# Optimization experiments

Measured on AMD Instinct MI355X. Metric: run time of the kernel, lower is better.

Reference implementation:

```python
import jax, jax.numpy as jnp
import numpy as np

L, B, N, D, H, DH, MLP = 4, 4, 2048, 512, 8, 64, 2048
EPS = 1e-5


def layer_norm(x, w, b):
    mu = jnp.mean(x, axis=-1, keepdims=True)
    var = jnp.mean(jnp.square(x - mu), axis=-1, keepdims=True)
    return (x - mu) * jax.lax.rsqrt(var + EPS) * w + b


def setup_inputs() -> dict:
    key = jax.random.key(0)
    ks = jax.random.split(key, 8)
    x = jax.random.normal(ks[0], (B, N, D), dtype=jnp.float32)
    # mask == 1.0 means blocked: triu(ones) - eye -> strict upper triangle
    mask = jnp.triu(jnp.ones((N, N), dtype=jnp.float32)) - jnp.eye(N, dtype=jnp.float32)
    s = 0.02
    return {
        "x": x,
        "mask": mask,
        "ln1_w": jnp.ones((L, D), jnp.float32),
        "ln1_b": jnp.zeros((L, D), jnp.float32),
        "w_qkv": jax.random.normal(ks[1], (L, D, 3 * H * DH), jnp.float32) * s,
        "w_out": jax.random.normal(ks[2], (L, H * DH, D), jnp.float32) * s,
        "b_out": jnp.zeros((L, D), jnp.float32),
        "ln2_w": jnp.ones((L, D), jnp.float32),
        "ln2_b": jnp.zeros((L, D), jnp.float32),
        "w1": jax.random.normal(ks[3], (L, D, MLP), jnp.float32) * s,
        "b1": jnp.zeros((L, MLP), jnp.float32),
        "w2": jax.random.normal(ks[4], (L, MLP, D), jnp.float32) * s,
        "b2": jnp.zeros((L, D), jnp.float32),
    }


def reference(x, mask, ln1_w, ln1_b, w_qkv, w_out, b_out, ln2_w, ln2_b, w1, b1, w2, b2):
    scale = DH ** (-0.5)
    blocked = (mask == 1.0)  # [N, N]
    for l in range(L):
        # --- masked self-attention (pre-norm) ---
        h = layer_norm(x, ln1_w[l], ln1_b[l])
        qkv = h @ w_qkv[l]                               # [B, N, 3*H*DH]
        q, k, v = jnp.split(qkv, 3, axis=-1)
        q = q.reshape(B, N, H, DH).transpose(0, 2, 1, 3)  # bhnd
        k = k.reshape(B, N, H, DH).transpose(0, 2, 1, 3)
        v = v.reshape(B, N, H, DH).transpose(0, 2, 1, 3)
        scores = jnp.einsum('bhnd,bhmd->bhnm', q, k) * scale
        scores = jnp.where(blocked, -jnp.inf, scores)
        att = jax.nn.softmax(scores, axis=-1)
        o = jnp.einsum('bhnm,bhmd->bhnd', att, v)
        o = o.transpose(0, 2, 1, 3).reshape(B, N, H * DH)
        x = x + (o @ w_out[l] + b_out[l])
        # --- GELU MLP (pre-norm) ---
        h2 = layer_norm(x, ln2_w[l], ln2_b[l])
        ff = jax.nn.gelu(h2 @ w1[l] + b1[l], approximate=False) @ w2[l] + b2[l]
        x = x + ff
    return x
```

## Files before the change

kernel.cpp:

```cpp
#include <hip/hip_runtime.h>
#include <math.h>

#define L 4
#define BATCH 4
#define N 2048
#define D 512
#define H 8
#define DH 64
#define MLPD 2048
#define M_ROWS (BATCH * N)
#define VTP 2064

using v8s = __attribute__((ext_vector_type(8))) short;
using v4f = __attribute__((ext_vector_type(4))) float;

__device__ inline short f2bf(float f) {
  union { float f; unsigned u; } v; v.f = f;
  unsigned r = v.u + 0x7FFFu + ((v.u >> 16) & 1u);
  return (short)(r >> 16);
}
__device__ inline unsigned pack2bf_t(float a, float b) {
  union { float f; unsigned u; } x, y; x.f = a; y.f = b;
  return (x.u >> 16) | (y.u & 0xFFFF0000u);
}

#define MFMA(a, b, c) __builtin_amdgcn_mfma_f32_16x16x32_bf16(a, b, c, 0, 0, 0)

__device__ __forceinline__ void gload_lds16(const void* g, void* l) {
  __builtin_amdgcn_global_load_lds((const __attribute__((address_space(1))) void*)g,
                                   (__attribute__((address_space(3))) void*)l, 16, 0, 0);
}

#define FENCE asm volatile("" ::: "memory")
#define BAR  do { FENCE; __builtin_amdgcn_s_barrier(); FENCE; } while (0)
#define VMW(n) asm volatile("s_waitcnt vmcnt(" #n ")" ::: "memory")

__global__ void copyf4_kernel(const float4* __restrict__ in, float4* __restrict__ out, int n) {
  int i = blockIdx.x * blockDim.x + threadIdx.x;
  if (i < n) out[i] = in[i];
}

__launch_bounds__(256)
__global__ void transpose_w_kernel(const float* __restrict__ src, short* __restrict__ dst,
                                   int R, int C, int qcols) {
  __shared__ float tile[32][33];
  const size_t base = (size_t)blockIdx.z * R * C;
  const int c0 = blockIdx.x * 32, r0 = blockIdx.y * 32;
  const int tx = threadIdx.x & 31, ty = threadIdx.x >> 5;
  #pragma unroll
  for (int i = ty; i < 32; i += 8)
    tile[i][tx] = src[base + (size_t)(r0 + i) * C + c0 + tx];
  __syncthreads();
  #pragma unroll
  for (int i = ty; i < 32; i += 8) {
    float val = tile[tx][i];
    if (c0 + i < qcols) val *= 0.125f;
    dst[base + (size_t)(c0 + i) * R + r0 + tx] = f2bf(val);
  }
}

__launch_bounds__(256)
__global__ void ln_kernel(const float* __restrict__ x, const float* __restrict__ w,
                          const float* __restrict__ b, short* __restrict__ out) {
  const int row = blockIdx.x * 4 + (threadIdx.x >> 6);
  const int lane = threadIdx.x & 63;
  const float* xr = x + (size_t)row * D;
  float4 a0 = *(const float4*)(xr + lane * 8);
  float4 a1 = *(const float4*)(xr + lane * 8 + 4);
  float v[8] = {a0.x, a0.y, a0.z, a0.w, a1.x, a1.y, a1.z, a1.w};
  float s = 0.f;
  #pragma unroll
  for (int j = 0; j < 8; ++j) s += v[j];
  #pragma unroll
  for (int m = 1; m < 64; m <<= 1) s += __shfl_xor(s, m, 64);
  const float mean = s * (1.0f / D);
  float q = 0.f;
  #pragma unroll
  for (int j = 0; j < 8; ++j) { float d = v[j] - mean; q += d * d; }
  #pragma unroll
  for (int m = 1; m < 64; m <<= 1) q += __shfl_xor(q, m, 64);
  const float rstd = rsqrtf(q * (1.0f / D) + 1e-5f);
  float4 w0 = *(const float4*)(w + lane * 8);
  float4 w1 = *(const float4*)(w + lane * 8 + 4);
  float4 b0 = *(const float4*)(b + lane * 8);
  float4 b1 = *(const float4*)(b + lane * 8 + 4);
  float wv[8] = {w0.x, w0.y, w0.z, w0.w, w1.x, w1.y, w1.z, w1.w};
  float bv[8] = {b0.x, b0.y, b0.z, b0.w, b1.x, b1.y, b1.z, b1.w};
  v8s r;
  #pragma unroll
  for (int j = 0; j < 8; ++j) r[j] = f2bf((v[j] - mean) * rstd * wv[j] + bv[j]);
  *(v8s*)(out + (size_t)row * D + lane * 8) = r;
}

template <int MODE, int NT>
__launch_bounds__(512, 2)
__global__ void gemm256_kernel(const short* __restrict__ A, const short* __restrict__ Bt,
                               const float* __restrict__ bias, void* __restrict__ Out,
                               short* __restrict__ Vt, int M, int Nc) {
  constexpr int K = NT * 64;
  __shared__ __align__(16) short Ah[4][128 * 64];
  __shared__ __align__(16) short Bh[4][128 * 64];
  const int tid = threadIdx.x, lane = tid & 63, w = tid >> 6;
  const int wr = w >> 2, wc = w & 3;
  const int r16 = lane & 15, g = lane >> 4;

  const int nxb = Nc >> 8;
  const int nyb = M >> 8;
  const int bid = (int)blockIdx.x;
  const int xcd = bid & 7, ii = bid >> 3;
  const int byi = xcd * (nyb >> 3) + ii / nxb;
  const int bxi = ii % nxb;
  const int m0 = byi << 8, n0 = bxi << 8;

  const int srow = lane >> 3;
  const int ssw = ((lane & 7) ^ srow) * 8;

  const short* Abase = A + (size_t)(m0 + srow) * K + ssw;
  const short* Bbase = Bt + (size_t)(n0 + srow) * K + ssw;

  auto STAGE_A = [&](int j) {
    const int jc = (j > 2 * NT - 1) ? (2 * NT - 1) : j;
    const int slot = j & 3, k0 = (jc >> 1) * 64, r0 = (jc & 1) * 128;
    #pragma unroll
    for (int i = 0; i < 2; ++i) {
      const int rr = i * 64 + w * 8;
      gload_lds16(Abase + (size_t)(r0 + rr) * K + k0, (char*)&Ah[slot][0] + rr * 128);
    }
  };
  auto STAGE_B = [&](int j) {
    const int jc = (j > 2 * NT - 1) ? (2 * NT - 1) : j;
    const int slot = j & 3, k0 = (jc >> 1) * 64, c0 = (jc & 1) * 128;
    #pragma unroll
    for (int i = 0; i < 2; ++i) {
      const int rr = i * 64 + w * 8;
      gload_lds16(Bbase + (size_t)(c0 + rr) * K + k0, (char*)&Bh[slot][0] + rr * 128);
    }
  };

  const int arow = wr * 64 + r16;
  const int brow = wc * 32 + r16;
  const int swz7 = r16 & 7;

  v8s ar[4][2], br0[2][2], br1[2][2];
  auto LDA = [&](int slot) {
    const char* base = (const char*)&Ah[slot][0];
    #pragma unroll
    for (int mf = 0; mf < 4; ++mf)
      #pragma unroll
      for (int kh = 0; kh < 2; ++kh)
        ar[mf][kh] = *(const v8s*)(base + (arow + mf * 16) * 128 + (((kh * 4 + g) ^ swz7) * 16));
  };
  auto LDB0 = [&](int slot) {
    const char* base = (const char*)&Bh[slot][0];
    #pragma unroll
    for (int nf = 0; nf < 2; ++nf)
      #pragma unroll
      for (int kh = 0; kh < 2; ++kh)
        br0[nf][kh] = *(const v8s*)(base + (brow + nf * 16) * 128 + (((kh * 4 + g) ^ swz7) * 16));
  };
  auto LDB1 = [&](int slot) {
    const char* base = (const char*)&Bh[slot][0];
    #pragma unroll
    for (int nf = 0; nf < 2; ++nf)
      #pragma unroll
      for (int kh = 0; kh < 2; ++kh)
        br1[nf][kh] = *(const v8s*)(base + (brow + nf * 16) * 128 + (((kh * 4 + g) ^ swz7) * 16));
  };

  v4f acc[2][2][4][2] = {};

#define MMA_Q(QM, QN, BR)                                                      \
  do {                                                                         \
    __builtin_amdgcn_s_setprio(1);                                             \
    _Pragma("unroll")                                                          \
    for (int kh = 0; kh < 2; ++kh)                                             \
      _Pragma("unroll")                                                        \
      for (int mf = 0; mf < 4; ++mf)                                           \
        _Pragma("unroll")                                                      \
        for (int nf = 0; nf < 2; ++nf)                                         \
          acc[QM][QN][mf][nf] = MFMA(ar[mf][kh], BR[nf][kh], acc[QM][QN][mf][nf]); \
    __builtin_amdgcn_s_setprio(0);                                             \
  } while (0)

  STAGE_A(0); STAGE_B(0); STAGE_B(1); STAGE_A(1); STAGE_A(2); STAGE_B(2); STAGE_B(3);
  VMW(6);
  BAR;

  auto KTILE = [&](int T, int sa) {
    LDA(sa); LDB0(sa);
    STAGE_A(2 * T + 3);
    BAR;
    MMA_Q(0, 0, br0);
    BAR;
    LDB1(sa + 1);
    BAR;
    MMA_Q(0, 1, br1);
    BAR;
    LDA(sa + 1);
    STAGE_A(2 * T + 4); STAGE_B(2 * T + 4);
    BAR;
    MMA_Q(1, 1, br1);
    BAR;
    STAGE_B(2 * T + 5);
    BAR;
    MMA_Q(1, 0, br0);
    VMW(6);
    BAR;
  };

  #pragma unroll
  for (int t2 = 0; t2 < NT / 2; ++t2) {
    KTILE(2 * t2, 0);
    KTILE(2 * t2 + 1, 2);
  }
#undef MMA_Q

  if constexpr (MODE == 3) {
    if (n0 >= 1024) {
      const int bb = m0 >> 11;
      const int cperm = 16 * (g >> 1) + 8 * (g & 1);
      #pragma unroll
      for (int qm = 0; qm < 2; ++qm)
        #pragma unroll
        for (int mf = 0; mf < 4; ++mf) {
          const int key0 = m0 + qm * 128 + wr * 64 + mf * 16;
          const int ng = (key0 & 2047) & ~63;
          const int ccol = 32 * (mf >> 1) + cperm + 4 * (mf & 1);
          #pragma unroll
          for (int qn = 0; qn < 2; ++qn)
            #pragma unroll
            for (int nf = 0; nf < 2; ++nf) {
              const int col = n0 + qn * 128 + wc * 32 + nf * 16 + r16;
              const int dhg = col - 1024;
              const int bh = bb * 8 + (dhg >> 6);
              short* dst = Vt + (size_t)(bh * 64 + (dhg & 63)) * VTP + ng + ccol;
              uint2 st;
              st.x = (unsigned)(unsigned short)f2bf(acc[qm][qn][mf][nf][0]) |
                     ((unsigned)(unsigned short)f2bf(acc[qm][qn][mf][nf][1]) << 16);
              st.y = (unsigned)(unsigned short)f2bf(acc[qm][qn][mf][nf][2]) |
                     ((unsigned)(unsigned short)f2bf(acc[qm][qn][mf][nf][3]) << 16);
              *(uint2*)dst = st;
            }
        }
      return;
    }
  }
  #pragma unroll
  for (int qm = 0; qm < 2; ++qm)
    #pragma unroll
    for (int mf = 0; mf < 4; ++mf) {
      const int row = m0 + qm * 128 + wr * 64 + mf * 16 + g * 4;
      #pragma unroll
      for (int qn = 0; qn < 2; ++qn)
        #pragma unroll
        for (int nf = 0; nf < 2; ++nf) {
          const int col = n0 + qn * 128 + wc * 32 + nf * 16 + r16;
          float bv = 0.0f;
          if constexpr (MODE == 1) bv = bias[col];
          #pragma unroll
          for (int r = 0; r < 4; ++r) {
            float val = acc[qm][qn][mf][nf][r] + bv;
            if constexpr (MODE == 1) {
              const float z = val * 0.70710678118f;
              const float az = fabsf(z);
              const float t = 1.0f / (1.0f + 0.3275911f * az);
              const float p =
                  0.254829592f +
                  t * (-0.284496736f + t * (1.421413741f + t * (-1.453152027f + t * 1.061405429f)));
              float er = 1.0f - p * t * __expf(-az * az);
              er = (z < 0.0f) ? -er : er;
              val = 0.5f * val * (1.0f + er);
            }
            ((short*)Out)[(size_t)(row + r) * Nc + col] = f2bf(val);
          }
        }
    }
}

template <int MODE, int BN>
__launch_bounds__(256)
__global__ void gemm128_kernel(const short* __restrict__ A, const short* __restrict__ Bt,
                               const float* __restrict__ bias, const float* __restrict__ Xres,
                               void* __restrict__ Out, int M, int Nc, int K) {
  constexpr int MR = (BN == 128) ? 4 : 2;
  __shared__ __align__(16) short As[2][128 * 64];
  __shared__ __align__(16) short Bs[2][BN * 64];
  const int tid = threadIdx.x;
  const int lane = tid & 63;
  const int w = tid >> 6;
  const int wr = (BN == 128) ? (w >> 1) : w;
  const int wc = (BN == 128) ? (w & 1) : 0;
  const int r16 = lane & 15, g = lane >> 4;

  const int nxb = Nc / BN;
  const int nyb = M >> 7;
  const int bid = (int)blockIdx.x;
  const int xcd = bid & 7;
  const int ii = bid >> 3;
  const int byi = xcd * (nyb >> 3) + ii / nxb;
  const int bxi = ii % nxb;
  const int m0 = byi * 128, n0 = bxi * BN;

  const int srow = lane >> 3;
  const int ssw = ((lane & 7) ^ srow) * 8;

  auto STAGE = [&](int buf, int k0) {
    #pragma unroll
    for (int j = 0; j < 4; ++j) {
      const int row = w * 32 + j * 8;
      gload_lds16(A + (size_t)(m0 + row + srow) * K + k0 + ssw,
                  (char*)&As[buf][0] + row * 128);
    }
    #pragma unroll
    for (int j = 0; j < BN / 32; ++j) {
      const int row = w * (BN / 4) + j * 8;
      gload_lds16(Bt + (size_t)(n0 + row + srow) * K + k0 + ssw,
                  (char*)&Bs[buf][0] + row * 128);
    }
  };

  v4f acc[MR][4] = {};

  STAGE(0, 0);
  __syncthreads();
  int cur = 0;
  for (int k0 = 0; k0 < K; k0 += 64) {
    if (k0 + 64 < K) STAGE(cur ^ 1, k0 + 64);
    v8s af[MR][2], bf[4][2];
    #pragma unroll
    for (int m = 0; m < MR; ++m) {
      const int row = wr * (MR * 16) + m * 16 + r16;
      #pragma unroll
      for (int kh = 0; kh < 2; ++kh)
        af[m][kh] = *(const v8s*)((const char*)&As[cur][0] + row * 128 +
                                  (((kh * 4 + g) ^ (row & 7)) * 16));
    }
    #pragma unroll
    for (int n = 0; n < 4; ++n) {
      const int row = wc * 64 + n * 16 + r16;
      #pragma unroll
      for (int kh = 0; kh < 2; ++kh)
        bf[n][kh] = *(const v8s*)((const char*)&Bs[cur][0] + row * 128 +
                                  (((kh * 4 + g) ^ (row & 7)) * 16));
    }
    #pragma unroll
    for (int kh = 0; kh < 2; ++kh)
      #pragma unroll
      for (int m = 0; m < MR; ++m)
        #pragma unroll
        for (int n = 0; n < 4; ++n)
          acc[m][n] = MFMA(af[m][kh], bf[n][kh], acc[m][n]);
    __syncthreads();
    cur ^= 1;
  }

  #pragma unroll
  for (int m = 0; m < MR; ++m) {
    const int row = m0 + wr * (MR * 16) + m * 16 + g * 4;
    #pragma unroll
    for (int n = 0; n < 4; ++n) {
      const int col = n0 + wc * 64 + n * 16 + r16;
      const float bv = bias ? bias[col] : 0.0f;
      #pragma unroll
      for (int r = 0; r < 4; ++r) {
        const size_t idx = (size_t)(row + r) * Nc + col;
        float val = acc[m][n][r] + bv;
        if constexpr (MODE == 0) {
          ((short*)Out)[idx] = f2bf(val);
        } else if constexpr (MODE == 1) {
          const float z = val * 0.70710678118f;
          const float az = fabsf(z);
          const float t = 1.0f / (1.0f + 0.3275911f * az);
          const float p =
              0.254829592f +
              t * (-0.284496736f + t * (1.421413741f + t * (-1.453152027f + t * 1.061405429f)));
          float er = 1.0f - p * t * __expf(-az * az);
          er = (z < 0.0f) ? -er : er;
          val = 0.5f * val * (1.0f + er);
          ((short*)Out)[idx] = f2bf(val);
        } else {
          ((float*)Out)[idx] = val + Xres[idx];
        }
      }
    }
  }
}

__launch_bounds__(256)
__global__ void attn_kernel(const short* __restrict__ qkv, const short* __restrict__ Vt,
                            short* __restrict__ o) {
  __shared__ __align__(16) short Ks[3][64 * 64];
  __shared__ __align__(16) short Vs[2][64 * 64];
  const int lin = (int)blockIdx.x;
  const int xcd = lin & 7;
  const int kk = lin >> 3;
  const int bh = (kk & 3) * 8 + xcd;
  const int xl = (kk < 32) ? (15 - (kk >> 2)) : ((kk - 32) >> 2);
  const int b = bh >> 3, h = bh & 7;
  const int q0 = xl * 128;
  const int tid = threadIdx.x, lane = tid & 63, w = tid >> 6;
  const int r16 = lane & 15, g = lane >> 4;
  const int qw = q0 + w * 32;

  v8s qa0, qa1, qb0, qb1;
  {
    const size_t qA = ((size_t)(b * N + qw + r16)) * 1536 + h * 64;
    const size_t qB = ((size_t)(b * N + qw + 16 + r16)) * 1536 + h * 64;
    qa0 = *(const v8s*)(qkv + qA + g * 8);
    qa1 = *(const v8s*)(qkv + qA + 32 + g * 8);
    qb0 = *(const v8s*)(qkv + qB + g * 8);
    qb1 = *(const v8s*)(qkv + qB + 32 + g * 8);
  }

  const short* vtb = Vt + (size_t)bh * 64 * VTP;

  const int srow = lane >> 3;
  const int ssw = ((lane & 7) ^ srow) * 8;

  v4f oaccA[4] = {}, oaccB[4] = {};
  float lsumA = 0.f, lsumB = 0.f;
  const int tdiag = 2 * xl + 1;
  const int wlast = 2 * xl + (w >> 1);
  const int nt = 2 * xl + 2;

  auto STAGE_K = [&](int t) {
    t = (t > tdiag) ? tdiag : t;
    const int k0 = t * 64, buf = t % 3;
    #pragma unroll
    for (int j = 0; j < 2; ++j) {
      const int row = w * 16 + j * 8;
      gload_lds16(qkv + ((size_t)(b * N + k0 + row + srow)) * 1536 + 512 + h * 64 + ssw,
                  (char*)&Ks[buf][0] + row * 128);
    }
  };
  auto STAGE_V = [&](int t) {
    t = (t > tdiag) ? tdiag : t;
    const int k0 = t * 64, buf = t & 1;
    #pragma unroll
    for (int j = 0; j < 2; ++j) {
      const int row = w * 16 + j * 8;
      gload_lds16(vtb + (size_t)(row + srow) * VTP + k0 + ssw,
                  (char*)&Vs[buf][0] + row * 128);
    }
  };

  STAGE_K(0); STAGE_V(0); STAGE_K(1);

  for (int t = 0; t < nt; ++t) {
    VMW(2);
    BAR;
    STAGE_V(t + 1);
    STAGE_K(t + 2);

    if (t <= wlast) {
      const char* kb = (const char*)&Ks[t % 3][0];
      const char* vb = (const char*)&Vs[t & 1][0];

      v8s vf[4][2];
      #pragma unroll
      for (int a = 0; a < 4; ++a)
        #pragma unroll
        for (int c = 0; c < 2; ++c)
          vf[a][c] = *(const v8s*)(vb + (a * 16 + r16) * 128 + (((c * 4 + g) ^ (r16 & 7)) * 16));

      __builtin_amdgcn_s_setprio(1);
      v4f sA[4], sB[4];
      #pragma unroll
      for (int kt = 0; kt < 4; ++kt) {
        const int krow = (kt * 16 + r16) * 128;
        v8s kfa = *(const v8s*)(kb + krow + ((g ^ (r16 & 7)) * 16));
        v8s kfb = *(const v8s*)(kb + krow + (((4 + g) ^ (r16 & 7)) * 16));
        v4f ss = {};
        ss = MFMA(kfa, qa0, ss);
        ss = MFMA(kfb, qa1, ss);
        sA[kt] = ss;
        v4f tt = {};
        tt = MFMA(kfa, qb0, tt);
        tt = MFMA(kfb, qb1, tt);
        sB[kt] = tt;
      }
      __builtin_amdgcn_s_setprio(0);

      const bool needmask = (t == wlast);
      const int qrowA = qw + r16;
      const int qrowB = qw + 16 + r16;
      const int kbase = t * 64 + 4 * g;
      unsigned pwA[8], pwB[8];
      #pragma unroll
      for (int kt = 0; kt < 4; ++kt) {
        float eA[4], eB[4];
        #pragma unroll
        for (int r = 0; r < 4; ++r) {
          const int key = kbase + kt * 16 + r;
          float va = sA[kt][r], vb2 = sB[kt][r];
          if (needmask) {
            if (key > qrowA) va = -3e38f;
            if (key > qrowB) vb2 = -3e38f;
          }
          eA[r] = __expf(va);
          eB[r] = __expf(vb2);
        }
        lsumA += (eA[0] + eA[1]) + (eA[2] + eA[3]);
        lsumB += (eB[0] + eB[1]) + (eB[2] + eB[3]);
        pwA[kt * 2 + 0] = pack2bf_t(eA[0], eA[1]);
        pwA[kt * 2 + 1] = pack2bf_t(eA[2], eA[3]);
        pwB[kt * 2 + 0] = pack2bf_t(eB[0], eB[1]);
        pwB[kt * 2 + 1] = pack2bf_t(eB[2], eB[3]);
      }
      union PU { unsigned u[4]; v8s s8; };
      PU pA0, pA1, pB0, pB1;
      pA0.u[0] = pwA[0]; pA0.u[1] = pwA[1]; pA0.u[2] = pwA[2]; pA0.u[3] = pwA[3];
      pA1.u[0] = pwA[4]; pA1.u[1] = pwA[5]; pA1.u[2] = pwA[6]; pA1.u[3] = pwA[7];
      pB0.u[0] = pwB[0]; pB0.u[1] = pwB[1]; pB0.u[2] = pwB[2]; pB0.u[3] = pwB[3];
      pB1.u[0] = pwB[4]; pB1.u[1] = pwB[5]; pB1.u[2] = pwB[6]; pB1.u[3] = pwB[7];

      __builtin_amdgcn_s_setprio(1);
      #pragma unroll
      for (int dt = 0; dt < 4; ++dt) {
        oaccA[dt] = MFMA(pA0.s8, vf[dt][0], oaccA[dt]);
        oaccB[dt] = MFMA(pB0.s8, vf[dt][0], oaccB[dt]);
      }
      #pragma unroll
      for (int dt = 0; dt < 4; ++dt) {
        oaccA[dt] = MFMA(pA1.s8, vf[dt][1], oaccA[dt]);
        oaccB[dt] = MFMA(pB1.s8, vf[dt][1], oaccB[dt]);
      }
      __builtin_amdgcn_s_setprio(0);
    }
  }

  lsumA += __shfl_xor(lsumA, 16, 64);
  lsumA += __shfl_xor(lsumA, 32, 64);
  lsumB += __shfl_xor(lsumB, 16, 64);
  lsumB += __shfl_xor(lsumB, 32, 64);
  const float linvA = 1.0f / lsumA;
  const float linvB = 1.0f / lsumB;
  float ldA[4], ldB[4];
  #pragma unroll
  for (int r = 0; r < 4; ++r) {
    ldA[r] = __shfl(linvA, g * 4 + r, 64);
    ldB[r] = __shfl(linvB, g * 4 + r, 64);
  }

  #pragma unroll
  for (int dt = 0; dt < 4; ++dt)
    #pragma unroll
    for (int r = 0; r < 4; ++r) {
      o[((size_t)(b * N + qw + g * 4 + r)) * 512 + h * 64 + dt * 16 + r16] =
          f2bf(oaccA[dt][r] * ldA[r]);
      o[((size_t)(b * N + qw + 16 + g * 4 + r)) * 512 + h * 64 + dt * 16 + r16] =
          f2bf(oaccB[dt][r] * ldB[r]);
    }
}

extern "C" void kernel_launch(void* const* d_in, const int* in_sizes, int n_in,
                              void* d_out, int out_size, void* d_ws, size_t ws_size,
                              hipStream_t stream) {
  const float* x_in  = (const float*)d_in[0];
  const float* ln1_w = (const float*)d_in[2];
  const float* ln1_b = (const float*)d_in[3];
  const float* w_qkv = (const float*)d_in[4];
  const float* w_out = (const float*)d_in[5];
  const float* b_out = (const float*)d_in[6];
  const float* ln2_w = (const float*)d_in[7];
  const float* ln2_b = (const float*)d_in[8];
  const float* w1    = (const float*)d_in[9];
  const float* b1    = (const float*)d_in[10];
  const float* w2    = (const float*)d_in[11];
  const float* b2    = (const float*)d_in[12];

  char* ws = (char*)d_ws;
  size_t off = 0;
  auto alloc = [&](size_t bytes) { char* p = ws + off; off += (bytes + 255) & ~(size_t)255; return p; };
  short* wqkvT = (short*)alloc((size_t)L * 1536 * 512 * 2);
  short* woutT = (short*)alloc((size_t)L * 512 * 512 * 2);
  short* w1T   = (short*)alloc((size_t)L * 512 * 2048 * 2);
  short* w2T   = (short*)alloc((size_t)L * 2048 * 512 * 2);
  short* hln   = (short*)alloc((size_t)M_ROWS * 512 * 2);
  short* big   = (short*)alloc((size_t)M_ROWS * 2048 * 2);
  short* oatt  = (short*)alloc((size_t)M_ROWS * 512 * 2);
  short* Vtg   = (short*)alloc((size_t)BATCH * H * 64 * VTP * 2);
  short* qkv = big;
  short* ff  = big;

  float* x = (float*)d_out;

  copyf4_kernel<<<4096, 256, 0, stream>>>((const float4*)x_in, (float4*)x, M_ROWS * D / 4);

  transpose_w_kernel<<<dim3(1536 / 32, 512 / 32, L), 256, 0, stream>>>(w_qkv, wqkvT, 512, 1536, 512);
  transpose_w_kernel<<<dim3(512 / 32, 512 / 32, L), 256, 0, stream>>>(w_out, woutT, 512, 512, 0);
  transpose_w_kernel<<<dim3(2048 / 32, 512 / 32, L), 256, 0, stream>>>(w1, w1T, 512, 2048, 0);
  transpose_w_kernel<<<dim3(512 / 32, 2048 / 32, L), 256, 0, stream>>>(w2, w2T, 2048, 512, 0);

  for (int l = 0; l < L; ++l) {
    ln_kernel<<<M_ROWS / 4, 256, 0, stream>>>(x, ln1_w + l * 512, ln1_b + l * 512, hln);
    gemm256_kernel<3, 8><<<dim3((1536 / 256) * (M_ROWS / 256)), 512, 0, stream>>>(
        hln, wqkvT + (size_t)l * 1536 * 512, nullptr, qkv, Vtg, M_ROWS, 1536);
    attn_kernel<<<dim3(512), 256, 0, stream>>>(qkv, Vtg, oatt);
    gemm128_kernel<2, 64><<<dim3((512 / 64) * (M_ROWS / 128)), 256, 0, stream>>>(
        oatt, woutT + (size_t)l * 512 * 512, b_out + l * 512, x, x, M_ROWS, 512, 512);
    ln_kernel<<<M_ROWS / 4, 256, 0, stream>>>(x, ln2_w + l * 512, ln2_b + l * 512, hln);
    gemm256_kernel<1, 8><<<dim3((2048 / 256) * (M_ROWS / 256)), 512, 0, stream>>>(
        hln, w1T + (size_t)l * 512 * 2048, b1 + l * 2048, ff, nullptr, M_ROWS, 2048);
    gemm128_kernel<2, 64><<<dim3((512 / 64) * (M_ROWS / 128)), 256, 0, stream>>>(
        ff, w2T + (size_t)l * 2048 * 512, b2 + l * 512, x, x, M_ROWS, 512, 2048);
  }
}
```

Measured before the change: 666.6 us.

## Split attention key tiles across wave pairs and drop initial input copy

The attention kernel now gives each block 64 query rows instead of 128 and launches twice as many blocks. Within a block, two wave pairs each handle half of every 64-key tile, and their partial outputs and row sums are merged through LDS at the end. This aims to balance the causal workload and raise occupancy, at the cost of an extra LDS reduction and two barriers. Separately, the upfront copy of x into the output buffer is removed: the first layer reads x_in directly for its layernorm and residual add.

```diff
diff --git a/kernel.cpp b/kernel.cpp
--- a/kernel.cpp
+++ b/kernel.cpp
@@ -34,11 +34,6 @@
 #define FENCE asm volatile("" ::: "memory")
 #define BAR  do { FENCE; __builtin_amdgcn_s_barrier(); FENCE; } while (0)
 #define VMW(n) asm volatile("s_waitcnt vmcnt(" #n ")" ::: "memory")
-
-__global__ void copyf4_kernel(const float4* __restrict__ in, float4* __restrict__ out, int n) {
-  int i = blockIdx.x * blockDim.x + threadIdx.x;
-  if (i < n) out[i] = in[i];
-}
 
 __launch_bounds__(256)
 __global__ void transpose_w_kernel(const float* __restrict__ src, short* __restrict__ dst,
@@ -392,15 +387,15 @@
   __shared__ __align__(16) short Ks[3][64 * 64];
   __shared__ __align__(16) short Vs[2][64 * 64];
   const int lin = (int)blockIdx.x;
-  const int xcd = lin & 7;
-  const int kk = lin >> 3;
-  const int bh = (kk & 3) * 8 + xcd;
-  const int xl = (kk < 32) ? (15 - (kk >> 2)) : ((kk - 32) >> 2);
+  const int bh = ((lin >> 3) & 3) * 8 + (lin & 7);
+  const int xl2 = 31 - (lin >> 5);
   const int b = bh >> 3, h = bh & 7;
-  const int q0 = xl * 128;
+  const int q0 = xl2 * 64;
   const int tid = threadIdx.x, lane = tid & 63, w = tid >> 6;
   const int r16 = lane & 15, g = lane >> 4;
-  const int qw = q0 + w * 32;
+  const int qw = q0 + (w & 1) * 32;
+  const int ko = (w >> 1) * 32;
+  const int kc = w >> 1;
 
   v8s qa0, qa1, qb0, qb1;
   {
@@ -419,9 +414,7 @@
 
   v4f oaccA[4] = {}, oaccB[4] = {};
   float lsumA = 0.f, lsumB = 0.f;
-  const int tdiag = 2 * xl + 1;
-  const int wlast = 2 * xl + (w >> 1);
-  const int nt = 2 * xl + 2;
+  const int tdiag = xl2;
 
   auto STAGE_K = [&](int t) {
     t = (t > tdiag) ? tdiag : t;
@@ -446,111 +439,127 @@
 
   STAGE_K(0); STAGE_V(0); STAGE_K(1);
 
-  for (int t = 0; t < nt; ++t) {
+  for (int t = 0; t <= tdiag; ++t) {
     VMW(2);
     BAR;
     STAGE_V(t + 1);
     STAGE_K(t + 2);
 
-    if (t <= wlast) {
-      const char* kb = (const char*)&Ks[t % 3][0];
-      const char* vb = (const char*)&Vs[t & 1][0];
-
-      v8s vf[4][2];
-      #pragma unroll
-      for (int a = 0; a < 4; ++a)
-        #pragma unroll
-        for (int c = 0; c < 2; ++c)
-          vf[a][c] = *(const v8s*)(vb + (a * 16 + r16) * 128 + (((c * 4 + g) ^ (r16 & 7)) * 16));
-
-      __builtin_amdgcn_s_setprio(1);
-      v4f sA[4], sB[4];
-      #pragma unroll
-      for (int kt = 0; kt < 4; ++kt) {
-        const int krow = (kt * 16 + r16) * 128;
-        v8s kfa = *(const v8s*)(kb + krow + ((g ^ (r16 & 7)) * 16));
-        v8s kfb = *(const v8s*)(kb + krow + (((4 + g) ^ (r16 & 7)) * 16));
-        v4f ss = {};
-        ss = MFMA(kfa, qa0, ss);
-        ss = MFMA(kfb, qa1, ss);
-        sA[kt] = ss;
-        v4f tt = {};
-        tt = MFMA(kfa, qb0, tt);
-        tt = MFMA(kfb, qb1, tt);
-        sB[kt] = tt;
+    const char* kb = (const char*)&Ks[t % 3][0];
+    const char* vb = (const char*)&Vs[t & 1][0];
+
+    v8s vf[4];
+    #pragma unroll
+    for (int a = 0; a < 4; ++a)
+      vf[a] = *(const v8s*)(vb + (a * 16 + r16) * 128 + (((kc * 4 + g) ^ (r16 & 7)) * 16));
+
+    __builtin_amdgcn_s_setprio(1);
+    v4f sA[2], sB[2];
+    #pragma unroll
+    for (int kt = 0; kt < 2; ++kt) {
+      const int krow = (ko + kt * 16 + r16) * 128;
+      v8s kfa = *(const v8s*)(kb + krow + ((g ^ (r16 & 7)) * 16));
+      v8s kfb = *(const v8s*)(kb + krow + (((4 + g) ^ (r16 & 7)) * 16));
+      v4f ss = {};
+      ss = MFMA(kfa, qa0, ss);
+      ss = MFMA(kfb, qa1, ss);
+      sA[kt] = ss;
+      v4f st = {};
+      st = MFMA(kfa, qb0, st);
+      st = MFMA(kfb, qb1, st);
+      sB[kt] = st;
+    }
+    __builtin_amdgcn_s_setprio(0);
+
+    const bool needmask = (t == tdiag);
+    const int qrowA = qw + r16;
+    const int qrowB = qw + 16 + r16;
+    const int kbase = t * 64 + ko + 4 * g;
+    unsigned pwA[4], pwB[4];
+    #pragma unroll
+    for (int kt = 0; kt < 2; ++kt) {
+      float eA[4], eB[4];
+      #pragma unroll
+      for (int r = 0; r < 4; ++r) {
+        const int key = kbase + kt * 16 + r;
+        float va = sA[kt][r], vb2 = sB[kt][r];
+        if (needmask) {
+          if (key > qrowA) va = -3e38f;
+          if (key > qrowB) vb2 = -3e38f;
+        }
+        eA[r] = __expf(va);
+        eB[r] = __expf(vb2);
       }
-      __builtin_amdgcn_s_setprio(0);
-
-      const bool needmask = (t == wlast);
-      const int qrowA = qw + r16;
-      const int qrowB = qw + 16 + r16;
-      const int kbase = t * 64 + 4 * g;
-      unsigned pwA[8], pwB[8];
-      #pragma unroll
-      for (int kt = 0; kt < 4; ++kt) {
-        float eA[4], eB[4];
-        #pragma unroll
-        for (int r = 0; r < 4; ++r) {
-          const int key = kbase + kt * 16 + r;
-          float va = sA[kt][r], vb2 = sB[kt][r];
-          if (needmask) {
-            if (key > qrowA) va = -3e38f;
-            if (key > qrowB) vb2 = -3e38f;
-          }
-          eA[r] = __expf(va);
-          eB[r] = __expf(vb2);
-        }
-        lsumA += (eA[0] + eA[1]) + (eA[2] + eA[3]);
-        lsumB += (eB[0] + eB[1]) + (eB[2] + eB[3]);
-        pwA[kt * 2 + 0] = pack2bf_t(eA[0], eA[1]);
-        pwA[kt * 2 + 1] = pack2bf_t(eA[2], eA[3]);
-        pwB[kt * 2 + 0] = pack2bf_t(eB[0], eB[1]);
-        pwB[kt * 2 + 1] = pack2bf_t(eB[2], eB[3]);
+      lsumA += (eA[0] + eA[1]) + (eA[2] + eA[3]);
+      lsumB += (eB[0] + eB[1]) + (eB[2] + eB[3]);
+      pwA[kt * 2 + 0] = pack2bf_t(eA[0], eA[1]);
+      pwA[kt * 2 + 1] = pack2bf_t(eA[2], eA[3]);
+      pwB[kt * 2 + 0] = pack2bf_t(eB[0], eB[1]);
+      pwB[kt * 2 + 1] = pack2bf_t(eB[2], eB[3]);
+    }
+    union PU { unsigned u[4]; v8s s8; };
+    PU pA, pB;
+    pA.u[0] = pwA[0]; pA.u[1] = pwA[1]; pA.u[2] = pwA[2]; pA.u[3] = pwA[3];
+    pB.u[0] = pwB[0]; pB.u[1] = pwB[1]; pB.u[2] = pwB[2]; pB.u[3] = pwB[3];
+
+    __builtin_amdgcn_s_setprio(1);
+    #pragma unroll
+    for (int dt = 0; dt < 4; ++dt) {
+      oaccA[dt] = MFMA(pA.s8, vf[dt], oaccA[dt]);
+      oaccB[dt] = MFMA(pB.s8, vf[dt], oaccB[dt]);
+    }
+    __builtin_amdgcn_s_setprio(0);
+  }
+
+  float* red = (float*)&Ks[0][0];
+  BAR;
+  if (w >= 2) {
+    float* mine = red + (size_t)(w - 2) * (64 * 34) + lane * 34;
+    #pragma unroll
+    for (int dt = 0; dt < 4; ++dt)
+      #pragma unroll
+      for (int r = 0; r < 4; ++r) {
+        mine[dt * 4 + r] = oaccA[dt][r];
+        mine[16 + dt * 4 + r] = oaccB[dt][r];
       }
-      union PU { unsigned u[4]; v8s s8; };
-      PU pA0, pA1, pB0, pB1;
-      pA0.u[0] = pwA[0]; pA0.u[1] = pwA[1]; pA0.u[2] = pwA[2]; pA0.u[3] = pwA[3];
-      pA1.u[0] = pwA[4]; pA1.u[1] = pwA[5]; pA1.u[2] = pwA[6]; pA1.u[3] = pwA[7];
-      pB0.u[0] = pwB[0]; pB0.u[1] = pwB[1]; pB0.u[2] = pwB[2]; pB0.u[3] = pwB[3];
-      pB1.u[0] = pwB[4]; pB1.u[1] = pwB[5]; pB1.u[2] = pwB[6]; pB1.u[3] = pwB[7];
-
-      __builtin_amdgcn_s_setprio(1);
-      #pragma unroll
-      for (int dt = 0; dt < 4; ++dt) {
-        oaccA[dt] = MFMA(pA0.s8, vf[dt][0], oaccA[dt]);
-        oaccB[dt] = MFMA(pB0.s8, vf[dt][0], oaccB[dt]);
+    mine[32] = lsumA;
+    mine[33] = lsumB;
+  }
+  BAR;
+  if (w < 2) {
+    const float* p = red + (size_t)w * (64 * 34) + lane * 34;
+    #pragma unroll
+    for (int dt = 0; dt < 4; ++dt)
+      #pragma unroll
+      for (int r = 0; r < 4; ++r) {
+        oaccA[dt][r] += p[dt * 4 + r];
+        oaccB[dt][r] += p[16 + dt * 4 + r];
       }
-      #pragma unroll
-      for (int dt = 0; dt < 4; ++dt) {
-        oaccA[dt] = MFMA(pA1.s8, vf[dt][1], oaccA[dt]);
-        oaccB[dt] = MFMA(pB1.s8, vf[dt][1], oaccB[dt]);
+    lsumA += p[32];
+    lsumB += p[33];
+
+    lsumA += __shfl_xor(lsumA, 16, 64);
+    lsumA += __shfl_xor(lsumA, 32, 64);
+    lsumB += __shfl_xor(lsumB, 16, 64);
+    lsumB += __shfl_xor(lsumB, 32, 64);
+    const float linvA = 1.0f / lsumA;
+    const float linvB = 1.0f / lsumB;
+    float ldA[4], ldB[4];
+    #pragma unroll
+    for (int r = 0; r < 4; ++r) {
+      ldA[r] = __shfl(linvA, g * 4 + r, 64);
+      ldB[r] = __shfl(linvB, g * 4 + r, 64);
+    }
+    #pragma unroll
+    for (int dt = 0; dt < 4; ++dt)
+      #pragma unroll
+      for (int r = 0; r < 4; ++r) {
+        o[((size_t)(b * N + qw + g * 4 + r)) * 512 + h * 64 + dt * 16 + r16] =
+            f2bf(oaccA[dt][r] * ldA[r]);
+        o[((size_t)(b * N + qw + 16 + g * 4 + r)) * 512 + h * 64 + dt * 16 + r16] =
+            f2bf(oaccB[dt][r] * ldB[r]);
       }
-      __builtin_amdgcn_s_setprio(0);
-    }
-  }
-
-  lsumA += __shfl_xor(lsumA, 16, 64);
-  lsumA += __shfl_xor(lsumA, 32, 64);
-  lsumB += __shfl_xor(lsumB, 16, 64);
-  lsumB += __shfl_xor(lsumB, 32, 64);
-  const float linvA = 1.0f / lsumA;
-  const float linvB = 1.0f / lsumB;
-  float ldA[4], ldB[4];
-  #pragma unroll
-  for (int r = 0; r < 4; ++r) {
-    ldA[r] = __shfl(linvA, g * 4 + r, 64);
-    ldB[r] = __shfl(linvB, g * 4 + r, 64);
-  }
-
-  #pragma unroll
-  for (int dt = 0; dt < 4; ++dt)
-    #pragma unroll
-    for (int r = 0; r < 4; ++r) {
-      o[((size_t)(b * N + qw + g * 4 + r)) * 512 + h * 64 + dt * 16 + r16] =
-          f2bf(oaccA[dt][r] * ldA[r]);
-      o[((size_t)(b * N + qw + 16 + g * 4 + r)) * 512 + h * 64 + dt * 16 + r16] =
-          f2bf(oaccB[dt][r] * ldB[r]);
-    }
+  }
 }
 
 extern "C" void kernel_launch(void* const* d_in, const int* in_sizes, int n_in,
@@ -585,20 +594,19 @@
 
   float* x = (float*)d_out;
 
-  copyf4_kernel<<<4096, 256, 0, stream>>>((const float4*)x_in, (float4*)x, M_ROWS * D / 4);
-
   transpose_w_kernel<<<dim3(1536 / 32, 512 / 32, L), 256, 0, stream>>>(w_qkv, wqkvT, 512, 1536, 512);
   transpose_w_kernel<<<dim3(512 / 32, 512 / 32, L), 256, 0, stream>>>(w_out, woutT, 512, 512, 0);
   transpose_w_kernel<<<dim3(2048 / 32, 512 / 32, L), 256, 0, stream>>>(w1, w1T, 512, 2048, 0);
   transpose_w_kernel<<<dim3(512 / 32, 2048 / 32, L), 256, 0, stream>>>(w2, w2T, 2048, 512, 0);
 
   for (int l = 0; l < L; ++l) {
-    ln_kernel<<<M_ROWS / 4, 256, 0, stream>>>(x, ln1_w + l * 512, ln1_b + l * 512, hln);
+    const float* xl = (l == 0) ? x_in : x;
+    ln_kernel<<<M_ROWS / 4, 256, 0, stream>>>(xl, ln1_w + l * 512, ln1_b + l * 512, hln);
     gemm256_kernel<3, 8><<<dim3((1536 / 256) * (M_ROWS / 256)), 512, 0, stream>>>(
         hln, wqkvT + (size_t)l * 1536 * 512, nullptr, qkv, Vtg, M_ROWS, 1536);
-    attn_kernel<<<dim3(512), 256, 0, stream>>>(qkv, Vtg, oatt);
+    attn_kernel<<<dim3(1024), 256, 0, stream>>>(qkv, Vtg, oatt);
     gemm128_kernel<2, 64><<<dim3((512 / 64) * (M_ROWS / 128)), 256, 0, stream>>>(
-        oatt, woutT + (size_t)l * 512 * 512, b_out + l * 512, x, x, M_ROWS, 512, 512);
+        oatt, woutT + (size_t)l * 512 * 512, b_out + l * 512, xl, x, M_ROWS, 512, 512);
     ln_kernel<<<M_ROWS / 4, 256, 0, stream>>>(x, ln2_w + l * 512, ln2_b + l * 512, hln);
     gemm256_kernel<1, 8><<<dim3((2048 / 256) * (M_ROWS / 256)), 512, 0, stream>>>(
         hln, w1T + (size_t)l * 512 * 2048, b1 + l * 2048, ff, nullptr, M_ROWS, 2048);
```

Result: faster. 592.0 us (-11.2%).
